# Kernel optimization log

Hardware: AMD Instinct MI355X
Metric: run time of the kernel (lower is better)

The kernel has to match this reference:

```python
import jax, jax.numpy as jnp
import numpy as np
from jax import lax

N_ITER = 50  # entmax-bisect iterations (entmax library default)
DEG = 12    # neighbors per node in global item graph


def entmax_bisect(X, alpha):
    # entmax with per-row alpha, over axis=1. X: [B, L, 1], alpha: [B, 1, 1]
    d = X.shape[1]
    Xa = X * (alpha - 1.0)
    inv = 1.0 / (alpha - 1.0)
    _p = lambda z: jnp.maximum(z, 0.0) ** inv
    max_val = jnp.max(Xa, axis=1, keepdims=True)
    tau_lo = max_val - 1.0                                   # _gp(1, alpha) = 1
    tau_hi = max_val - jnp.power(1.0 / d, alpha - 1.0)       # _gp(1/d, alpha)
    f_lo = jnp.sum(_p(Xa - tau_lo), axis=1, keepdims=True) - 1.0

    def body(i, carry):
        tau_lo, dm, _ = carry
        dm = dm * 0.5
        tau_m = tau_lo + dm
        f_m = jnp.sum(_p(Xa - tau_m), axis=1, keepdims=True) - 1.0
        tau_lo = jnp.where(f_m * f_lo >= 0.0, tau_m, tau_lo)
        return (tau_lo, dm, tau_m)

    tau_lo, dm, tau_m = lax.fori_loop(0, N_ITER, body, (tau_lo, tau_hi - tau_lo, tau_lo))
    p_m = _p(Xa - tau_m)
    return p_m / jnp.sum(p_m, axis=1, keepdims=True)  # ensure_sum_one


def setup_inputs() -> dict:
    key = jax.random.key(0)
    ks = jax.random.split(key, 10)
    B, L, D, N = 1024, 50, 256, 40000
    E = N * DEG
    stdv = 1.0 / np.sqrt(D)
    u = lambda k, shape: jax.random.uniform(k, shape, jnp.float32, -stdv, stdv)

    item_emb = u(ks[0], (N, D)).at[0].set(0.0)  # padding_idx=0
    items = jax.random.randint(ks[1], (B, L), 0, N)
    inputs_seq = jax.random.randint(ks[2], (B, L), 0, N)
    alias_inputs = jax.random.randint(ks[3], (B, L), 0, L)
    target_embedding = jax.random.normal(ks[4], (B, 1, 2 * D), jnp.float32)

    # sparse global item adjacency (row-normalized, DEG neighbors per node)
    adj_rows = jnp.repeat(jnp.arange(N, dtype=jnp.int32), DEG)
    adj_cols = jax.random.randint(ks[5], (E,), 0, N, dtype=jnp.int32)
    adj_vals = jax.random.uniform(ks[6], (E,), jnp.float32) / DEG

    kp = jax.random.split(ks[7], 10)
    return {
        "items": items, "inputs_seq": inputs_seq, "alias_inputs": alias_inputs,
        "target_embedding": target_embedding, "item_emb": item_emb,
        "adj_rows": adj_rows, "adj_cols": adj_cols, "adj_vals": adj_vals,
        "wf_w": u(kp[0], (D, 2 * D)), "wf_b": u(kp[1], (D,)),
        "alphaw_w": u(kp[2], (1, D)), "alphaw_b": u(kp[3], (1,)),
        "at_w0": u(kp[4], (1, D)), "at_w1": u(kp[5], (D, D)),
        "at_w2": u(kp[6], (D, D)), "at_bias": u(kp[7], (D,)),
    }


def reference(items, inputs_seq, alias_inputs, target_embedding, item_emb,
              adj_rows, adj_cols, adj_vals, wf_w, wf_b, alphaw_w, alphaw_b,
              at_w0, at_w1, at_w2, at_bias):
    N = item_emb.shape[0]
    # GlobalItemConv (1 layer): h = (x + adj @ x) / 2 via sparse SpMM
    agg = jax.ops.segment_sum(adj_vals[:, None] * item_emb[adj_cols], adj_rows,
                              num_segments=N)
    graph_embs = (item_emb + agg) * 0.5

    hidden = graph_embs[items]                              # [B, L, D] (dropout: eval)
    target_emb = target_embedding @ wf_w.T + wf_b           # [B, 1, D]

    # get_alpha: sigmoid + 1, then masked_fill(==1 -> 1.00001)
    alpha_ent = jax.nn.sigmoid(target_emb @ alphaw_w.T + alphaw_b) + 1.0  # [B,1,1]
    alpha_ent = jnp.where(alpha_ent == 1.0, 1.00001, alpha_ent)

    # tglobal_attention
    scores = jax.nn.relu(hidden @ at_w1 + target_emb @ at_w2 + at_bias) @ at_w0.T  # [B,L,1]
    attn = entmax_bisect(scores, alpha_ent)                 # sparse softmax over L
    c = jnp.einsum('blo,bld->bod', attn, hidden)[:, 0, :]   # alpha^T @ v, squeeze -> [B,D]

    c = jax.nn.selu(c)
    return c / jnp.linalg.norm(c, axis=-1, keepdims=True)
```

## Files before the change

### kernel.cpp

```cpp
#include <hip/hip_runtime.h>
#include <hip/hip_bf16.h>
#include <math.h>

#define BB 1024
#define LL 50
#define DD 256
#define TWO_D 512
#define NN 40000
#define DEG 12
#define NITER 50

typedef __attribute__((ext_vector_type(8))) short short8;
typedef __attribute__((ext_vector_type(4))) float floatx4;

__device__ __forceinline__ float wave_sum64(float v) {
#pragma unroll
    for (int off = 32; off > 0; off >>= 1) v += __shfl_xor(v, off, 64);
    return v;
}
__device__ __forceinline__ float wave_max64(float v) {
#pragma unroll
    for (int off = 32; off > 0; off >>= 1) v = fmaxf(v, __shfl_xor(v, off, 64));
    return v;
}
__device__ __forceinline__ float bf2f(ushort u) {
    union { unsigned int i; float f; } c; c.i = ((unsigned int)u) << 16; return c.f;
}
__device__ __forceinline__ ushort f2bf(float f) {
    __hip_bfloat16 h = __float2bfloat16(f);
    return *(ushort*)&h;
}
__device__ __forceinline__ float hw_exp2(float x) { return __builtin_amdgcn_exp2f(x); }
__device__ __forceinline__ float hw_log2(float x) { return __builtin_amdgcn_logf(x); }

__global__ __launch_bounds__(256) void k_stage1(
    const float* __restrict__ emb, ushort* __restrict__ ebf,
    const int* __restrict__ items, int* __restrict__ flags,
    const float* __restrict__ wf_w, const float* __restrict__ wf_b,
    const float* __restrict__ at_w2, const float* __restrict__ at_bias,
    const float* __restrict__ aw, const float* __restrict__ ab,
    const float* __restrict__ at_w1,
    float* __restrict__ Wc, float* __restrict__ v,
    float* __restrict__ bc, float* __restrict__ c0,
    ushort* __restrict__ w1t)
{
    __shared__ float wcol[DD];
    __shared__ float4 s_p[4][64];
    __shared__ float wred[4];
    __shared__ ushort s_t[4][DD];
    int bid = blockIdx.x;
    int tid = threadIdx.x;

    if (bid < 512) {
        int k = bid;
        int lane = tid & 63, wv = tid >> 6;
        int ng = tid & 63;
        int dq = tid >> 6;

        wcol[tid] = wf_w[tid * TWO_D + k];
        __syncthreads();

        float4 acc = {0.f, 0.f, 0.f, 0.f};
        const float4* w24 = (const float4*)at_w2;
#pragma unroll 8
        for (int d = dq * 64; d < dq * 64 + 64; ++d) {
            float4 w2 = w24[d * 64 + ng];
            float wc = wcol[d];
            acc.x += wc * w2.x; acc.y += wc * w2.y;
            acc.z += wc * w2.z; acc.w += wc * w2.w;
        }
        s_p[dq][ng] = acc;

        float s1 = wcol[tid] * aw[tid];
        s1 = wave_sum64(s1);
        if (lane == 0) wred[wv] = s1;
        __syncthreads();
        if (tid == 0) v[k] = wred[0] + wred[1] + wred[2] + wred[3];

        if (tid < 64) {
            float4 r0 = s_p[0][tid], r1 = s_p[1][tid];
            float4 r2 = s_p[2][tid], r3 = s_p[3][tid];
            float4 rr;
            rr.x = (r0.x + r1.x) + (r2.x + r3.x);
            rr.y = (r0.y + r1.y) + (r2.y + r3.y);
            rr.z = (r0.z + r1.z) + (r2.z + r3.z);
            rr.w = (r0.w + r1.w) + (r2.w + r3.w);
            *(float4*)(Wc + k * DD + tid * 4) = rr;
        }

        if (k < 64) {
            int k0 = k * 4;
#pragma unroll
            for (int j = 0; j < 4; ++j)
                s_t[j][tid] = f2bf(at_w1[(k0 + j) * DD + tid]);
            __syncthreads();
            ushort4 pk;
            pk.x = s_t[0][tid]; pk.y = s_t[1][tid];
            pk.z = s_t[2][tid]; pk.w = s_t[3][tid];
            *(ushort4*)(w1t + tid * DD + k0) = pk;
        }

        if (k == 0) {
            __syncthreads();
            wcol[tid] = wf_b[tid];
            __syncthreads();
            float b[8];
#pragma unroll
            for (int j = 0; j < 8; ++j) b[j] = 0.f;
#pragma unroll 4
            for (int d = 0; d < DD; d += 8) {
#pragma unroll
                for (int j = 0; j < 8; ++j)
                    b[j] += wcol[d + j] * at_w2[(d + j) * DD + tid];
            }
            bc[tid] = at_bias[tid] + ((b[0] + b[1]) + (b[2] + b[3]))
                                   + ((b[4] + b[5]) + (b[6] + b[7]));
            float s2 = wcol[tid] * aw[tid];
            s2 = wave_sum64(s2);
            if (lane == 0) wred[wv] = s2;
            __syncthreads();
            if (tid == 0) c0[0] = wred[0] + wred[1] + wred[2] + wred[3] + ab[0];
        }
    } else if (bid < 712) {
        int i = (bid - 512) * 256 + tid;
        flags[items[i]] = 1;
    } else {
        int base4 = (bid - 712) * (256 * 8) + tid;
        float4 val[8];
#pragma unroll
        for (int j = 0; j < 8; ++j)
            val[j] = *(const float4*)(emb + (size_t)(base4 + j * 256) * 4);
#pragma unroll
        for (int j = 0; j < 8; ++j) {
            ushort4 o;
            o.x = f2bf(val[j].x); o.y = f2bf(val[j].y);
            o.z = f2bf(val[j].z); o.w = f2bf(val[j].w);
            *(ushort4*)(ebf + (size_t)(base4 + j * 256) * 4) = o;
        }
    }
}

__global__ __launch_bounds__(256) void k_stage2(
    const ushort* __restrict__ ebf, const int* __restrict__ adj_cols,
    const float* __restrict__ adj_vals, const int* __restrict__ flags,
    ushort* __restrict__ gbf,
    const float* __restrict__ tgt, const float* __restrict__ Wc,
    const float* __restrict__ bc, const float* __restrict__ v,
    const float* __restrict__ c0, float* __restrict__ t2,
    float* __restrict__ alpha)
{
    __shared__ float x_s[4 * TWO_D];
    int bid = blockIdx.x;
    int tid = threadIdx.x;
    int wv = tid >> 6, lane = tid & 63;

    if (bid < 1024) {
        int t = bid;
        int btile = t >> 2, ntile = t & 3;
        int b0 = btile * 4, n0 = ntile * 64;
        int j = wv;
        for (int i = tid; i < 4 * TWO_D; i += 256) x_s[i] = tgt[b0 * TWO_D + i];
        __syncthreads();

        float acc = bc[n0 + lane];
        const float* xr = x_s + j * TWO_D;
#pragma unroll 8
        for (int k = 0; k < TWO_D; ++k)
            acc += xr[k] * Wc[k * DD + n0 + lane];
        t2[(b0 + j) * DD + n0 + lane] = acc;

        if (ntile == 0) {
            float s = 0.f;
#pragma unroll
            for (int i = 0; i < 8; ++i) s += xr[lane + 64 * i] * v[lane + 64 * i];
            s = wave_sum64(s);
            if (lane == 0) {
                float a = 1.f + 1.f / (1.f + expf(-(s + c0[0])));
                if (a == 1.f) a = 1.00001f;
                alpha[b0 + j] = a;
            }
        }
    } else {
        int n = (bid - 1024) * 4 + wv;
        if (flags[n] != 1) return;
        int colv = 0; float valv = 0.f;
        if (lane < DEG) { colv = adj_cols[n * DEG + lane]; valv = adj_vals[n * DEG + lane]; }
        int cols[DEG]; float vals[DEG];
#pragma unroll
        for (int k = 0; k < DEG; ++k) {
            cols[k] = __shfl(colv, k, 64);
            vals[k] = __shfl(valv, k, 64);
        }
        ushort4 s = *(const ushort4*)(ebf + (size_t)n * DD + lane * 4);
        ushort4 e[DEG];
#pragma unroll
        for (int k = 0; k < DEG; ++k)
            e[k] = *(const ushort4*)(ebf + (size_t)cols[k] * DD + lane * 4);
        float a0 = bf2f(s.x), a1 = bf2f(s.y), a2 = bf2f(s.z), a3 = bf2f(s.w);
#pragma unroll
        for (int k = 0; k < DEG; ++k) {
            float vv = vals[k];
            a0 += vv * bf2f(e[k].x); a1 += vv * bf2f(e[k].y);
            a2 += vv * bf2f(e[k].z); a3 += vv * bf2f(e[k].w);
        }
        ushort4 o;
        o.x = f2bf(0.5f * a0); o.y = f2bf(0.5f * a1);
        o.z = f2bf(0.5f * a2); o.w = f2bf(0.5f * a3);
        *(ushort4*)(gbf + (size_t)n * DD + lane * 4) = o;
    }
}

__global__ __launch_bounds__(256, 2) void k_scores_mfma(
    const int* __restrict__ items, const ushort* __restrict__ gbf,
    const ushort* __restrict__ w1t, const float* __restrict__ t2,
    const float* __restrict__ at_w0, float* __restrict__ scores)
{
    __shared__ __align__(16) ushort sA[128 * 72];
    __shared__ __align__(16) ushort sB[256 * 72];
    __shared__ float sred[128][4];
    __shared__ int s_items[128];
    int tid = threadIdx.x;
    int blk = blockIdx.x;
    int lane = tid & 63, wv = tid >> 6;
    int cn = lane & 15, q = lane >> 4;
    int n0 = wv * 64;

    if (tid < 128) s_items[tid] = items[blk * 128 + tid];
    __syncthreads();

    floatx4 acc[8][4];
#pragma unroll
    for (int mt = 0; mt < 8; ++mt)
#pragma unroll
        for (int nt = 0; nt < 4; ++nt)
            acc[mt][nt] = (floatx4){0.f, 0.f, 0.f, 0.f};

#pragma unroll 1
    for (int kc = 0; kc < 4; ++kc) {
#pragma unroll
        for (int it = 0; it < 4; ++it) {
            int i = tid + it * 256;
            int row = i >> 3, seg = i & 7;
            *(uint4*)(sA + row * 72 + seg * 8) =
                *(const uint4*)(gbf + (size_t)s_items[row] * DD + kc * 64 + seg * 8);
        }
#pragma unroll
        for (int it = 0; it < 8; ++it) {
            int i = tid + it * 256;
            int n = i >> 3, seg = i & 7;
            *(uint4*)(sB + n * 72 + seg * 8) =
                *(const uint4*)(w1t + n * DD + kc * 64 + seg * 8);
        }
        __syncthreads();
#pragma unroll
        for (int ks = 0; ks < 2; ++ks) {
            short8 af[8], bfr[4];
#pragma unroll
            for (int mt = 0; mt < 8; ++mt)
                af[mt] = *(const short8*)(sA + (mt * 16 + cn) * 72 + ks * 32 + q * 8);
#pragma unroll
            for (int nt = 0; nt < 4; ++nt)
                bfr[nt] = *(const short8*)(sB + (n0 + nt * 16 + cn) * 72 + ks * 32 + q * 8);
#pragma unroll
            for (int mt = 0; mt < 8; ++mt)
#pragma unroll
                for (int nt = 0; nt < 4; ++nt)
                    acc[mt][nt] = __builtin_amdgcn_mfma_f32_16x16x32_bf16(
                        af[mt], bfr[nt], acc[mt][nt], 0, 0, 0);
        }
        __syncthreads();
    }

    float w0v[4];
#pragma unroll
    for (int nt = 0; nt < 4; ++nt) w0v[nt] = at_w0[n0 + nt * 16 + cn];
#pragma unroll
    for (int mt = 0; mt < 8; ++mt) {
#pragma unroll
        for (int r = 0; r < 4; ++r) {
            int row_in = q * 4 + r;
            int row = mt * 16 + row_in;
            int b = (blk * 128 + row) / LL;
            const float* t2b = t2 + b * DD;
            float p = 0.f;
#pragma unroll
            for (int nt = 0; nt < 4; ++nt) {
                int col = n0 + nt * 16 + cn;
                float vv = acc[mt][nt][r] + t2b[col];
                p += fmaxf(vv, 0.f) * w0v[nt];
            }
            p += __shfl_xor(p, 1, 64);
            p += __shfl_xor(p, 2, 64);
            p += __shfl_xor(p, 4, 64);
            p += __shfl_xor(p, 8, 64);
            if (cn == 0) sred[row][wv] = p;
        }
    }
    __syncthreads();
    if (tid < 128)
        scores[blk * 128 + tid] = sred[tid][0] + sred[tid][1] + sred[tid][2] + sred[tid][3];
}

__device__ __forceinline__ float pw(float z, float invv) {
    return hw_exp2(invv * hw_log2(z));
}

__global__ __launch_bounds__(256) void k_entmax_out(
    const float* __restrict__ scores, const float* __restrict__ alpha,
    const int* __restrict__ items, const ushort* __restrict__ gbf,
    float* __restrict__ out)
{
    __shared__ float attn_s[LL];
    __shared__ int s_it[LL];
    __shared__ float red[4];
    int b = blockIdx.x;
    int tid = threadIdx.x;

    if (tid >= 192 && tid < 192 + LL) s_it[tid - 192] = items[b * LL + (tid - 192)];

    if (tid < 64) {
        int l = tid;
        float a = alpha[b];
        float am1 = a - 1.f;
        float invv = 1.f / am1;
        float x = (l < LL) ? scores[b * LL + l] : -__builtin_inff();
        float Xa = x * am1;

        float mx = wave_max64(Xa);
        float tau_lo = mx - 1.f;
        float tau_hi = mx - hw_exp2(am1 * hw_log2(1.f / (float)LL));

        float f_lo = wave_sum64(pw(fmaxf(Xa - tau_lo, 0.f), invv)) - 1.f;

        float dm = tau_hi - tau_lo;
        float tau_m = tau_lo;
#pragma unroll 1
        for (int it = 0; it < NITER; ++it) {
            dm *= 0.5f;
            tau_m = tau_lo + dm;
            if (tau_m == tau_lo) break;
            float f_m = wave_sum64(pw(fmaxf(Xa - tau_m, 0.f), invv)) - 1.f;
            if (f_m * f_lo >= 0.f) tau_lo = tau_m;
        }
        float pm = pw(fmaxf(Xa - tau_m, 0.f), invv);
        float s = wave_sum64(pm);
        if (l < LL) attn_s[l] = pm / s;
    }
    __syncthreads();

    int d = tid;
    float c = 0.f;
#pragma unroll
    for (int l = 0; l < LL; ++l)
        c += attn_s[l] * bf2f(gbf[(size_t)s_it[l] * DD + d]);

    const float SC = 1.0507009873554805f;
    const float AL = 1.6732632423543772f;
    c = SC * (c > 0.f ? c : AL * expm1f(c));

    float ss = wave_sum64(c * c);
    int wv = tid >> 6, lane = tid & 63;
    if (lane == 0) red[wv] = ss;
    __syncthreads();
    float tot = red[0] + red[1] + red[2] + red[3];
    out[b * DD + d] = c / sqrtf(tot);
}

extern "C" void kernel_launch(void* const* d_in, const int* in_sizes, int n_in,
                              void* d_out, int out_size, void* d_ws, size_t ws_size,
                              hipStream_t stream) {
    const int*   items     = (const int*)  d_in[0];
    const float* tgt       = (const float*)d_in[3];
    const float* item_emb  = (const float*)d_in[4];
    const int*   adj_cols  = (const int*)  d_in[6];
    const float* adj_vals  = (const float*)d_in[7];
    const float* wf_w      = (const float*)d_in[8];
    const float* wf_b      = (const float*)d_in[9];
    const float* alphaw_w  = (const float*)d_in[10];
    const float* alphaw_b  = (const float*)d_in[11];
    const float* at_w0     = (const float*)d_in[12];
    const float* at_w1     = (const float*)d_in[13];
    const float* at_w2     = (const float*)d_in[14];
    const float* at_bias   = (const float*)d_in[15];

    const size_t SZ_TAB = (size_t)NN * DD * sizeof(ushort);
    char* ws = (char*)d_ws;
    ushort* gbf = (ushort*)ws;   ws += SZ_TAB;
    ushort* ebf = (ushort*)ws;   ws += SZ_TAB;
    ushort* w1t = (ushort*)ws;   ws += (size_t)DD * DD * sizeof(ushort);
    int*   flags = (int*)ws;     ws += (size_t)NN * sizeof(int);
    float* Wc     = (float*)ws;  ws += (size_t)TWO_D * DD * sizeof(float);
    float* bcv    = (float*)ws;  ws += (size_t)DD * sizeof(float);
    float* vv     = (float*)ws;  ws += (size_t)TWO_D * sizeof(float);
    float* c0v    = (float*)ws;  ws += 16 * sizeof(float);
    float* t2     = (float*)ws;  ws += (size_t)BB * DD * sizeof(float);
    float* alpha  = (float*)ws;  ws += ((size_t)BB + 32) * sizeof(float);
    float* scores = (float*)ws;  ws += (size_t)BB * LL * sizeof(float);
    float* out    = (float*)d_out;

    k_stage1<<<1962, 256, 0, stream>>>(item_emb, ebf, items, flags,
                                       wf_w, wf_b, at_w2, at_bias,
                                       alphaw_w, alphaw_b, at_w1,
                                       Wc, vv, bcv, c0v, w1t);
    k_stage2<<<11024, 256, 0, stream>>>(ebf, adj_cols, adj_vals, flags, gbf,
                                        tgt, Wc, bcv, vv, c0v, t2, alpha);
    k_scores_mfma<<<(BB * LL) / 128, 256, 0, stream>>>(items, gbf, w1t, t2, at_w0, scores);
    k_entmax_out<<<BB, 256, 0, stream>>>(scores, alpha, items, gbf, out);
}
```

Before: 185.7 us.

## Fuse scores GEMM with entmax and output into one per-batch kernel

Merges the MFMA scoring kernel and the entmax/attention kernel into a single kernel with one block per batch row. The 50 gathered embedding rows are kept in shared memory and reused for the weighted sum, and t2 is staged in shared memory. This removes the scores round-trip through global memory, one launch, and the second gather of gbf rows. Wave reductions in the bisection loop switch to DPP, and the SpMM broadcast uses readlane. The cost is that each block now computes only 64 padded rows (50 valid), so MFMA tiles are smaller and the w1t tile is reloaded by 1024 blocks instead of 400.

New measurement: 183.4 us. About the same (-1.2%).

```diff
diff --git a/kernel.cpp b/kernel.cpp
--- a/kernel.cpp
+++ b/kernel.cpp
@@ -22,6 +22,18 @@
 #pragma unroll
     for (int off = 32; off > 0; off >>= 1) v = fmaxf(v, __shfl_xor(v, off, 64));
     return v;
+}
+__device__ __forceinline__ float dpp_sum64(float v) {
+#define DPPADD(ctrl, rm, bm) \
+    v += __int_as_float(__builtin_amdgcn_update_dpp(0, __float_as_int(v), ctrl, rm, bm, true))
+    DPPADD(0x111, 0xF, 0xF);
+    DPPADD(0x112, 0xF, 0xF);
+    DPPADD(0x114, 0xF, 0xE);
+    DPPADD(0x118, 0xF, 0xC);
+    DPPADD(0x142, 0xA, 0xF);
+    DPPADD(0x143, 0xC, 0xF);
+#undef DPPADD
+    return __int_as_float(__builtin_amdgcn_readlane(__float_as_int(v), 63));
 }
 __device__ __forceinline__ float bf2f(ushort u) {
     union { unsigned int i; float f; } c; c.i = ((unsigned int)u) << 16; return c.f;
@@ -188,8 +200,8 @@
         int cols[DEG]; float vals[DEG];
 #pragma unroll
         for (int k = 0; k < DEG; ++k) {
-            cols[k] = __shfl(colv, k, 64);
-            vals[k] = __shfl(valv, k, 64);
+            cols[k] = __builtin_amdgcn_readlane(colv, k);
+            vals[k] = __int_as_float(__builtin_amdgcn_readlane(__float_as_int(valv), k));
         }
         ushort4 s = *(const ushort4*)(ebf + (size_t)n * DD + lane * 4);
         ushort4 e[DEG];
@@ -210,40 +222,57 @@
     }
 }
 
-__global__ __launch_bounds__(256, 2) void k_scores_mfma(
+__device__ __forceinline__ float pw(float z, float invv) {
+    return hw_exp2(invv * hw_log2(z));
+}
+
+#define SA_LD 264
+
+__global__ __launch_bounds__(256, 2) void k_fused(
     const int* __restrict__ items, const ushort* __restrict__ gbf,
     const ushort* __restrict__ w1t, const float* __restrict__ t2,
-    const float* __restrict__ at_w0, float* __restrict__ scores)
+    const float* __restrict__ at_w0, const float* __restrict__ alpha,
+    float* __restrict__ out)
 {
-    __shared__ __align__(16) ushort sA[128 * 72];
+    __shared__ __align__(16) ushort sA[64 * SA_LD];
     __shared__ __align__(16) ushort sB[256 * 72];
-    __shared__ float sred[128][4];
-    __shared__ int s_items[128];
+    __shared__ float t2_s[DD];
+    __shared__ float sred[64][4];
+    __shared__ float scores_s[64];
+    __shared__ int s_items[64];
+    __shared__ float attn_s[64];
+    __shared__ float red[4];
+
+    int b = blockIdx.x;
     int tid = threadIdx.x;
-    int blk = blockIdx.x;
     int lane = tid & 63, wv = tid >> 6;
     int cn = lane & 15, q = lane >> 4;
     int n0 = wv * 64;
 
-    if (tid < 128) s_items[tid] = items[blk * 128 + tid];
+    if (tid < 64) {
+        int l = (tid < LL) ? tid : 0;
+        s_items[tid] = items[b * LL + l];
+    }
+    t2_s[tid] = t2[b * DD + tid];
     __syncthreads();
 
-    floatx4 acc[8][4];
-#pragma unroll
-    for (int mt = 0; mt < 8; ++mt)
+#pragma unroll
+    for (int it = 0; it < 8; ++it) {
+        int i = tid + it * 256;
+        int row = i >> 5, ch = i & 31;
+        *(uint4*)(sA + row * SA_LD + ch * 8) =
+            *(const uint4*)(gbf + (size_t)s_items[row] * DD + ch * 8);
+    }
+
+    floatx4 acc[4][4];
+#pragma unroll
+    for (int mt = 0; mt < 4; ++mt)
 #pragma unroll
         for (int nt = 0; nt < 4; ++nt)
             acc[mt][nt] = (floatx4){0.f, 0.f, 0.f, 0.f};
 
 #pragma unroll 1
     for (int kc = 0; kc < 4; ++kc) {
-#pragma unroll
-        for (int it = 0; it < 4; ++it) {
-            int i = tid + it * 256;
-            int row = i >> 3, seg = i & 7;
-            *(uint4*)(sA + row * 72 + seg * 8) =
-                *(const uint4*)(gbf + (size_t)s_items[row] * DD + kc * 64 + seg * 8);
-        }
 #pragma unroll
         for (int it = 0; it < 8; ++it) {
             int i = tid + it * 256;
@@ -254,15 +283,15 @@
         __syncthreads();
 #pragma unroll
         for (int ks = 0; ks < 2; ++ks) {
-            short8 af[8], bfr[4];
-#pragma unroll
-            for (int mt = 0; mt < 8; ++mt)
-                af[mt] = *(const short8*)(sA + (mt * 16 + cn) * 72 + ks * 32 + q * 8);
+            short8 af[4], bfr[4];
+#pragma unroll
+            for (int mt = 0; mt < 4; ++mt)
+                af[mt] = *(const short8*)(sA + (mt * 16 + cn) * SA_LD + kc * 64 + ks * 32 + q * 8);
 #pragma unroll
             for (int nt = 0; nt < 4; ++nt)
                 bfr[nt] = *(const short8*)(sB + (n0 + nt * 16 + cn) * 72 + ks * 32 + q * 8);
 #pragma unroll
-            for (int mt = 0; mt < 8; ++mt)
+            for (int mt = 0; mt < 4; ++mt)
 #pragma unroll
                 for (int nt = 0; nt < 4; ++nt)
                     acc[mt][nt] = __builtin_amdgcn_mfma_f32_16x16x32_bf16(
@@ -275,19 +304,16 @@
 #pragma unroll
     for (int nt = 0; nt < 4; ++nt) w0v[nt] = at_w0[n0 + nt * 16 + cn];
 #pragma unroll
-    for (int mt = 0; mt < 8; ++mt) {
+    for (int mt = 0; mt < 4; ++mt) {
 #pragma unroll
         for (int r = 0; r < 4; ++r) {
-            int row_in = q * 4 + r;
-            int row = mt * 16 + row_in;
-            int b = (blk * 128 + row) / LL;
-            const float* t2b = t2 + b * DD;
+            int row = mt * 16 + q * 4 + r;
             float p = 0.f;
 #pragma unroll
             for (int nt = 0; nt < 4; ++nt) {
                 int col = n0 + nt * 16 + cn;
-                float vv = acc[mt][nt][r] + t2b[col];
-                p += fmaxf(vv, 0.f) * w0v[nt];
+                float vvv = acc[mt][nt][r] + t2_s[col];
+                p += fmaxf(vvv, 0.f) * w0v[nt];
             }
             p += __shfl_xor(p, 1, 64);
             p += __shfl_xor(p, 2, 64);
@@ -297,40 +323,23 @@
         }
     }
     __syncthreads();
-    if (tid < 128)
-        scores[blk * 128 + tid] = sred[tid][0] + sred[tid][1] + sred[tid][2] + sred[tid][3];
-}
-
-__device__ __forceinline__ float pw(float z, float invv) {
-    return hw_exp2(invv * hw_log2(z));
-}
-
-__global__ __launch_bounds__(256) void k_entmax_out(
-    const float* __restrict__ scores, const float* __restrict__ alpha,
-    const int* __restrict__ items, const ushort* __restrict__ gbf,
-    float* __restrict__ out)
-{
-    __shared__ float attn_s[LL];
-    __shared__ int s_it[LL];
-    __shared__ float red[4];
-    int b = blockIdx.x;
-    int tid = threadIdx.x;
-
-    if (tid >= 192 && tid < 192 + LL) s_it[tid - 192] = items[b * LL + (tid - 192)];
+    if (tid < 64)
+        scores_s[tid] = sred[tid][0] + sred[tid][1] + sred[tid][2] + sred[tid][3];
+    __syncthreads();
 
     if (tid < 64) {
         int l = tid;
         float a = alpha[b];
         float am1 = a - 1.f;
         float invv = 1.f / am1;
-        float x = (l < LL) ? scores[b * LL + l] : -__builtin_inff();
+        float x = (l < LL) ? scores_s[l] : -__builtin_inff();
         float Xa = x * am1;
 
         float mx = wave_max64(Xa);
         float tau_lo = mx - 1.f;
         float tau_hi = mx - hw_exp2(am1 * hw_log2(1.f / (float)LL));
 
-        float f_lo = wave_sum64(pw(fmaxf(Xa - tau_lo, 0.f), invv)) - 1.f;
+        float f_lo = dpp_sum64(pw(fmaxf(Xa - tau_lo, 0.f), invv)) - 1.f;
 
         float dm = tau_hi - tau_lo;
         float tau_m = tau_lo;
@@ -339,27 +348,29 @@
             dm *= 0.5f;
             tau_m = tau_lo + dm;
             if (tau_m == tau_lo) break;
-            float f_m = wave_sum64(pw(fmaxf(Xa - tau_m, 0.f), invv)) - 1.f;
+            float f_m = dpp_sum64(pw(fmaxf(Xa - tau_m, 0.f), invv)) - 1.f;
             if (f_m * f_lo >= 0.f) tau_lo = tau_m;
         }
         float pm = pw(fmaxf(Xa - tau_m, 0.f), invv);
-        float s = wave_sum64(pm);
+        float s = dpp_sum64(pm);
         if (l < LL) attn_s[l] = pm / s;
     }
     __syncthreads();
 
     int d = tid;
-    float c = 0.f;
-#pragma unroll
-    for (int l = 0; l < LL; ++l)
-        c += attn_s[l] * bf2f(gbf[(size_t)s_it[l] * DD + d]);
+    float c0_ = 0.f, c1_ = 0.f;
+#pragma unroll
+    for (int l = 0; l < LL; l += 2) {
+        c0_ += attn_s[l]     * bf2f(sA[l * SA_LD + d]);
+        c1_ += attn_s[l + 1] * bf2f(sA[(l + 1) * SA_LD + d]);
+    }
+    float c = c0_ + c1_;
 
     const float SC = 1.0507009873554805f;
     const float AL = 1.6732632423543772f;
     c = SC * (c > 0.f ? c : AL * expm1f(c));
 
     float ss = wave_sum64(c * c);
-    int wv = tid >> 6, lane = tid & 63;
     if (lane == 0) red[wv] = ss;
     __syncthreads();
     float tot = red[0] + red[1] + red[2] + red[3];
@@ -395,7 +406,6 @@
     float* c0v    = (float*)ws;  ws += 16 * sizeof(float);
     float* t2     = (float*)ws;  ws += (size_t)BB * DD * sizeof(float);
     float* alpha  = (float*)ws;  ws += ((size_t)BB + 32) * sizeof(float);
-    float* scores = (float*)ws;  ws += (size_t)BB * LL * sizeof(float);
     float* out    = (float*)d_out;
 
     k_stage1<<<1962, 256, 0, stream>>>(item_emb, ebf, items, flags,
@@ -404,6 +414,5 @@
                                        Wc, vv, bcv, c0v, w1t);
     k_stage2<<<11024, 256, 0, stream>>>(ebf, adj_cols, adj_vals, flags, gbf,
                                         tgt, Wc, bcv, vv, c0v, t2, alpha);
-    k_scores_mfma<<<(BB * LL) / 128, 256, 0, stream>>>(items, gbf, w1t, t2, at_w0, scores);
-    k_entmax_out<<<BB, 256, 0, stream>>>(scores, alpha, items, gbf, out);
-}
+    k_fused<<<BB, 256, 0, stream>>>(items, gbf, w1t, t2, at_w0, alpha, out);
+}
```
